# Kernel optimization log

Measured on AMD Instinct MI355X. Metric: run time of the kernel, lower is better.

## Reference

```python
import jax, jax.numpy as jnp
import numpy as np

N0 = N1 = N2 = N3 = 8          # input_shape
R = 8                           # input_ranks (rank_i)
L = 8                           # link_ranks (ring bond dims)
OR = 64                         # output_rank
OF = 1024                       # output_features
B = 4096                        # batch
STD = 0.09                      # ~calculate_std() for this config


def setup_inputs() -> dict:
    key = jax.random.key(0)
    ks = jax.random.split(key, 9)
    x = jax.random.normal(ks[0], (B, N0, N1, N2, N3), dtype=jnp.float32)
    # factor_i: (n_i, link_left, link_right, rank_i)
    f0 = jax.random.normal(ks[1], (N0, L, L, R), dtype=jnp.float32) * STD
    f1 = jax.random.normal(ks[2], (N1, L, L, R), dtype=jnp.float32) * STD
    f2 = jax.random.normal(ks[3], (N2, L, L, R), dtype=jnp.float32) * STD
    f3 = jax.random.normal(ks[4], (N3, L, L, R), dtype=jnp.float32) * STD
    core = jax.random.normal(ks[5], (R, R, R, R, OR), dtype=jnp.float32) * STD
    out_factor = jax.random.normal(ks[6], (OR, OF), dtype=jnp.float32) * STD
    bound = 1.0 / np.sqrt(N0 * N1 * N2 * N3)
    bias = jax.random.uniform(ks[7], (OF,), dtype=jnp.float32, minval=-bound, maxval=bound)
    return {"x": x, "f0": f0, "f1": f1, "f2": f2, "f3": f3,
            "core": core, "out_factor": out_factor, "bias": bias}


def _tr_weight(f0, f1, f2, f3, core, out_factor):
    # Contract the tensor-ring (factors + core + output factor) into the
    # effective weight W[n0,n1,n2,n3,out]. Contraction order chosen so every
    # intermediate stays small; result equals tn.contractors.greedy output.
    # core axes: p=r0, q=r1, s=r2, t=r3, o=out_rank; links a,b,c,d close the ring.
    t1 = jnp.einsum('iabp,pqsto->iabqsto', f0, core)      # [n0,L,L,r1,r2,r3,or]
    t2 = jnp.einsum('jbcq,iabqsto->ijacsto', f1, t1)      # [n0,n1,L,L,r2,r3,or]
    t3 = jnp.einsum('kcds,ijacsto->ijkadto', f2, t2)      # [n0,n1,n2,L,L,r3,or]
    t4 = jnp.einsum('ldat,ijkadto->ijklo', f3, t3)        # ring trace -> [n0..n3,or]
    return jnp.einsum('ijklo,of->ijklf', t4, out_factor)  # [n0,n1,n2,n3,out]


def reference(x, f0, f1, f2, f3, core, out_factor, bias):
    W = _tr_weight(f0, f1, f2, f3, core, out_factor)      # [8,8,8,8,1024]
    out = jnp.einsum('bijkl,ijklf->bf', x, W)             # [B, out_features]
    return out + bias
```

## Files before the change

kernel.cpp:

```cpp
#include <hip/hip_runtime.h>


#define WS_NEED ((size_t)25231360 * 4)

typedef __attribute__((ext_vector_type(8))) short short8v;
typedef __attribute__((ext_vector_type(4))) float f32x4;

__device__ inline unsigned short f2bf(float f) {
  unsigned u = __builtin_bit_cast(unsigned, f);
  u += 0x7FFFu + ((u >> 16) & 1u);
  return (unsigned short)(u >> 16);
}
__device__ inline float bf2f(unsigned short h) {
  return __builtin_bit_cast(float, (unsigned)h << 16);
}


__global__ __launch_bounds__(256) void k_build(const float* __restrict__ f0,
                                               const float* __restrict__ f1,
                                               const float* __restrict__ f2,
                                               const float* __restrict__ f3,
                                               float* __restrict__ G01,
                                               float* __restrict__ G23) {
  int bb = blockIdx.x, tid = threadIdx.x;
  __shared__ float lu[512], lv[512];
  bool is01 = bb < 64;
  int pairi = is01 ? bb : bb - 64;
  int iA = pairi >> 3, iB = pairi & 7;
  const float* fu = is01 ? f0 : f2;
  const float* fv = is01 ? f1 : f3;
  if (tid < 128)
    reinterpret_cast<float4*>(lu)[tid] = reinterpret_cast<const float4*>(fu + iA * 512)[tid];
  else
    reinterpret_cast<float4*>(lv)[tid - 128] = reinterpret_cast<const float4*>(fv + iB * 512)[tid - 128];
  __syncthreads();
  float* dst = is01 ? G01 : G23;
#pragma unroll
  for (int r = 0; r < 16; ++r) {
    int idx = r * 256 + tid;
    int uv = idx >> 6, pq = idx & 63;
    int a = uv >> 3, c = uv & 7, p = pq >> 3, q = pq & 7;
    float acc = 0.f;
    if (is01) {
#pragma unroll
      for (int b = 0; b < 8; ++b)
        acc = fmaf(lu[a * 64 + b * 8 + p], lv[b * 64 + c * 8 + q], acc);
    } else {
#pragma unroll
      for (int d = 0; d < 8; ++d)
        acc = fmaf(lu[c * 64 + d * 8 + p], lv[d * 64 + a * 8 + q], acc);
    }
    dst[pairi * 4096 + idx] = acc;
  }
}


__global__ __launch_bounds__(256) void k_packs(const float* __restrict__ G01,
                                               const float* __restrict__ G23,
                                               const float* __restrict__ core,
                                               const float* __restrict__ OF_,
                                               unsigned short* __restrict__ G01p,
                                               unsigned short* __restrict__ CP,
                                               unsigned short* __restrict__ G23p,
                                               unsigned short* __restrict__ OFp) {
  int bb = blockIdx.x, tid = threadIdx.x;
  __shared__ float ls[8192];
  if (bb < 64) {
    int ij = bb;
#pragma unroll
    for (int r = 0; r < 4; ++r)
      reinterpret_cast<float4*>(ls)[r * 256 + tid] =
          reinterpret_cast<const float4*>(G01 + ij * 4096)[r * 256 + tid];
    __syncthreads();
    short8v* dst = reinterpret_cast<short8v*>(G01p);
#pragma unroll
    for (int it = 0; it < 2; ++it) {
      int item = it * 256 + tid;
      int ks = item >> 8, mf = (item >> 6) & 3, l = item & 63;
      short8v hi, lo;
#pragma unroll
      for (int j = 0; j < 8; ++j) {
        float v = ls[(mf * 16 + (l & 15)) * 64 + ks * 32 + 8 * (l >> 4) + j];
        unsigned short h = f2bf(v);
        hi[j] = (short)h; lo[j] = (short)f2bf(v - bf2f(h));
      }
      size_t base = ((((size_t)ij * 2 + ks) * 4 + mf) * 2) * 64 + l;
      dst[base] = hi; dst[base + 64] = lo;
    }
  } else if (bb < 128) {
    int st = bb - 64;
#pragma unroll
    for (int r = 0; r < 4; ++r) {
      int f4 = r * 256 + tid;
      reinterpret_cast<float4*>(ls)[f4] =
          reinterpret_cast<const float4*>(core)[(f4 >> 4) * 1024 + st * 16 + (f4 & 15)];
    }
    __syncthreads();
    short8v* dst = reinterpret_cast<short8v*>(CP);
#pragma unroll
    for (int it = 0; it < 2; ++it) {
      int item = it * 256 + tid;
      int ks = item >> 8, nf = (item >> 6) & 3, l = item & 63;
      short8v hi, lo;
#pragma unroll
      for (int j = 0; j < 8; ++j) {
        float v = ls[(ks * 32 + 8 * (l >> 4) + j) * 64 + nf * 16 + (l & 15)];
        unsigned short h = f2bf(v);
        hi[j] = (short)h; lo[j] = (short)f2bf(v - bf2f(h));
      }
      size_t base = ((((size_t)st * 2 + ks) * 4 + nf) * 2) * 64 + l;
      dst[base] = hi; dst[base + 64] = lo;
    }
  } else if (bb < 256) {
    int ks = bb - 128;
    int st = ks >> 1, acb = (ks & 1) * 32;
#pragma unroll
    for (int r = 0; r < 8; ++r) {
      int idx = r * 256 + tid;
      ls[idx] = G23[(idx >> 5) * 4096 + (acb + (idx & 31)) * 64 + st];
    }
    __syncthreads();
    short8v* dst = reinterpret_cast<short8v*>(G23p);
    int mf = tid >> 6, l = tid & 63;
    short8v hi, lo;
#pragma unroll
    for (int j = 0; j < 8; ++j) {
      float v = ls[(mf * 16 + (l & 15)) * 32 + 8 * (l >> 4) + j];
      unsigned short h = f2bf(v);
      hi[j] = (short)h; lo[j] = (short)f2bf(v - bf2f(h));
    }
    size_t base = (((size_t)ks * 4 + mf) * 2) * 64 + l;
    dst[base] = hi; dst[base + 64] = lo;
  } else {
    int g = bb - 256;
#pragma unroll
    for (int it = 0; it < 8; ++it) {
      int f4 = it * 256 + tid;
      reinterpret_cast<float4*>(ls)[f4] =
          reinterpret_cast<const float4*>(OF_)[(f4 >> 5) * 256 + g * 32 + (f4 & 31)];
    }
    __syncthreads();
    short8v* dst = reinterpret_cast<short8v*>(OFp);
#pragma unroll
    for (int it = 0; it < 4; ++it) {
      int item = it * 256 + tid;
      int nfl = item >> 7, ks = (item >> 6) & 1, l = item & 63;
      short8v hi, lo;
#pragma unroll
      for (int j = 0; j < 8; ++j) {
        float v = ls[(ks * 32 + 8 * (l >> 4) + j) * 128 + nfl * 16 + (l & 15)];
        unsigned short h = f2bf(v);
        hi[j] = (short)h; lo[j] = (short)f2bf(v - bf2f(h));
      }
      int nfg = g * 8 + nfl;
      size_t base = (((size_t)nfg * 2 + ks) * 2) * 64 + l;
      dst[base] = hi; dst[base + 64] = lo;
    }
  }
}


__global__ __launch_bounds__(256) void k_dmat(const unsigned short* __restrict__ G01p,
                                              const unsigned short* __restrict__ CP,
                                              unsigned short* __restrict__ Dp) {
  int bid = blockIdx.x;
  int ij = bid >> 6, st = bid & 63;
  int w = threadIdx.x >> 6, l = threadIdx.x & 63;
  const short8v* gp = reinterpret_cast<const short8v*>(G01p);
  const short8v* cp = reinterpret_cast<const short8v*>(CP);
  short8v ah0 = gp[((((size_t)ij * 2 + 0) * 4 + w) * 2) * 64 + l];
  short8v al0 = gp[((((size_t)ij * 2 + 0) * 4 + w) * 2) * 64 + 64 + l];
  short8v ah1 = gp[((((size_t)ij * 2 + 1) * 4 + w) * 2) * 64 + l];
  short8v al1 = gp[((((size_t)ij * 2 + 1) * 4 + w) * 2) * 64 + 64 + l];
  f32x4 acc[4];
#pragma unroll
  for (int nf = 0; nf < 4; ++nf) acc[nf] = (f32x4){0.f, 0.f, 0.f, 0.f};
#pragma unroll
  for (int nf = 0; nf < 4; ++nf) {
    short8v bh0 = cp[((((size_t)st * 2 + 0) * 4 + nf) * 2) * 64 + l];
    short8v bl0 = cp[((((size_t)st * 2 + 0) * 4 + nf) * 2) * 64 + 64 + l];
    short8v bh1 = cp[((((size_t)st * 2 + 1) * 4 + nf) * 2) * 64 + l];
    short8v bl1 = cp[((((size_t)st * 2 + 1) * 4 + nf) * 2) * 64 + 64 + l];
    acc[nf] = __builtin_amdgcn_mfma_f32_16x16x32_bf16(ah0, bh0, acc[nf], 0, 0, 0);
    acc[nf] = __builtin_amdgcn_mfma_f32_16x16x32_bf16(al0, bh0, acc[nf], 0, 0, 0);
    acc[nf] = __builtin_amdgcn_mfma_f32_16x16x32_bf16(ah0, bl0, acc[nf], 0, 0, 0);
    acc[nf] = __builtin_amdgcn_mfma_f32_16x16x32_bf16(ah1, bh1, acc[nf], 0, 0, 0);
    acc[nf] = __builtin_amdgcn_mfma_f32_16x16x32_bf16(al1, bh1, acc[nf], 0, 0, 0);
    acc[nf] = __builtin_amdgcn_mfma_f32_16x16x32_bf16(ah1, bl1, acc[nf], 0, 0, 0);
  }
  __shared__ float lds[64 * 66];
#pragma unroll
  for (int nf = 0; nf < 4; ++nf)
#pragma unroll
    for (int r = 0; r < 4; ++r)
      lds[(w * 16 + 4 * (l >> 4) + r) * 66 + nf * 16 + (l & 15)] = acc[nf][r];
  __syncthreads();
  short8v* dst = reinterpret_cast<short8v*>(Dp);
#pragma unroll
  for (int it = 0; it < 2; ++it) {
    int item = it * 256 + threadIdx.x;
    int a2 = item >> 8, nf = (item >> 6) & 3, l2 = item & 63;
    short8v hi, lo;
#pragma unroll
    for (int j = 0; j < 8; ++j) {
      float v = lds[(a2 * 32 + 8 * (l2 >> 4) + j) * 66 + nf * 16 + (l2 & 15)];
      unsigned short hh = f2bf(v);
      hi[j] = (short)hh; lo[j] = (short)f2bf(v - bf2f(hh));
    }
    int ks = st * 2 + a2;
    size_t base = ((((size_t)ij * 128 + ks) * 4 + nf) * 2) * 64 + l2;
    dst[base] = hi; dst[base + 64] = lo;
  }
}


__global__ __launch_bounds__(256) void k_t4mm(const unsigned short* __restrict__ G23p,
                                              const unsigned short* __restrict__ Dp,
                                              float* __restrict__ T4part) {
  int bid = blockIdx.x;
  int ij = bid >> 3, kc = bid & 7;
  int w = threadIdx.x >> 6, l = threadIdx.x & 63;
  const short8v* ga = reinterpret_cast<const short8v*>(G23p);
  const short8v* gb = reinterpret_cast<const short8v*>(Dp);
  f32x4 acc[4];
#pragma unroll
  for (int nf = 0; nf < 4; ++nf) acc[nf] = (f32x4){0.f, 0.f, 0.f, 0.f};
#pragma unroll 2
  for (int ks = kc * 16; ks < kc * 16 + 16; ++ks) {
    size_t abase = (((size_t)ks * 4 + w) * 2) * 64 + l;
    short8v ah = ga[abase], al = ga[abase + 64];
#pragma unroll
    for (int nf = 0; nf < 4; ++nf) {
      size_t bbase = ((((size_t)ij * 128 + ks) * 4 + nf) * 2) * 64 + l;
      short8v bh = gb[bbase], bl = gb[bbase + 64];
      acc[nf] = __builtin_amdgcn_mfma_f32_16x16x32_bf16(ah, bh, acc[nf], 0, 0, 0);
      acc[nf] = __builtin_amdgcn_mfma_f32_16x16x32_bf16(al, bh, acc[nf], 0, 0, 0);
      acc[nf] = __builtin_amdgcn_mfma_f32_16x16x32_bf16(ah, bl, acc[nf], 0, 0, 0);
    }
  }
#pragma unroll
  for (int nf = 0; nf < 4; ++nf)
#pragma unroll
    for (int r = 0; r < 4; ++r) {
      int row = w * 16 + 4 * (l >> 4) + r;
      T4part[(((size_t)kc * 64 + ij) * 64 + row) * 64 + nf * 16 + (l & 15)] = acc[nf][r];
    }
}


__global__ __launch_bounds__(256) void k_pack2(const float* __restrict__ T4part,
                                               unsigned short* __restrict__ Bp) {
  int kb = blockIdx.x, tid = threadIdx.x;
  __shared__ float ls[2048];
  f32x4 a0 = {0.f, 0.f, 0.f, 0.f}, a1 = a0;
#pragma unroll
  for (int kc = 0; kc < 8; ++kc) {
    const f32x4* src = reinterpret_cast<const f32x4*>(T4part + (size_t)kc * 262144 + kb * 2048);
    a0 += src[tid];
    a1 += src[256 + tid];
  }
  reinterpret_cast<f32x4*>(ls)[tid] = a0;
  reinterpret_cast<f32x4*>(ls)[256 + tid] = a1;
  __syncthreads();
  short8v* dst = reinterpret_cast<short8v*>(Bp);
  int nf = tid >> 6, l = tid & 63;
  short8v hi, lo;
#pragma unroll
  for (int j = 0; j < 8; ++j) {
    float v = ls[(8 * (l >> 4) + j) * 64 + nf * 16 + (l & 15)];
    unsigned short h = f2bf(v);
    hi[j] = (short)h; lo[j] = (short)f2bf(v - bf2f(h));
  }
  size_t base = (size_t)kb * 512 + (nf * 2) * 64 + l;
  dst[base] = hi; dst[base + 64] = lo;
}


__global__ __launch_bounds__(256) void k_ymm(const float* __restrict__ x,
                                             const unsigned short* __restrict__ Bp,
                                             float* __restrict__ Ypart) {
  int mt = blockIdx.x >> 4, kc = blockIdx.x & 15;
  int w = threadIdx.x >> 6, l = threadIdx.x & 63;
  int kg = l >> 4, lm = l & 15;
  const float4* xp = reinterpret_cast<const float4*>(
      x + (size_t)(mt * 64 + w * 16 + lm) * 4096 + kc * 256 + kg * 8);
  f32x4 acc0 = {0.f, 0.f, 0.f, 0.f}, acc1 = acc0, acc2 = acc0, acc3 = acc0;
#pragma unroll 1
  for (int s = 0; s < 8; ++s) {
    float4 xa = xp[s * 8], xb = xp[s * 8 + 1];
    float xs[8] = {xa.x, xa.y, xa.z, xa.w, xb.x, xb.y, xb.z, xb.w};
    short8v ah, al;
#pragma unroll
    for (int j = 0; j < 8; ++j) {
      unsigned u = __builtin_bit_cast(unsigned, xs[j]);
      unsigned short h = (unsigned short)(u >> 16);
      ah[j] = (short)h;
      float lo = xs[j] - bf2f(h);
      al[j] = (short)(__builtin_bit_cast(unsigned, lo) >> 16);
    }
    const short8v* bp = reinterpret_cast<const short8v*>(Bp + (size_t)(kc * 8 + s) * 4096) + l;
    short8v bh0 = bp[0],   bl0 = bp[64];
    short8v bh1 = bp[128], bl1 = bp[192];
    short8v bh2 = bp[256], bl2 = bp[320];
    short8v bh3 = bp[384], bl3 = bp[448];
    acc0 = __builtin_amdgcn_mfma_f32_16x16x32_bf16(ah, bh0, acc0, 0, 0, 0);
    acc1 = __builtin_amdgcn_mfma_f32_16x16x32_bf16(ah, bh1, acc1, 0, 0, 0);
    acc2 = __builtin_amdgcn_mfma_f32_16x16x32_bf16(ah, bh2, acc2, 0, 0, 0);
    acc3 = __builtin_amdgcn_mfma_f32_16x16x32_bf16(ah, bh3, acc3, 0, 0, 0);
    acc0 = __builtin_amdgcn_mfma_f32_16x16x32_bf16(al, bh0, acc0, 0, 0, 0);
    acc1 = __builtin_amdgcn_mfma_f32_16x16x32_bf16(al, bh1, acc1, 0, 0, 0);
    acc2 = __builtin_amdgcn_mfma_f32_16x16x32_bf16(al, bh2, acc2, 0, 0, 0);
    acc3 = __builtin_amdgcn_mfma_f32_16x16x32_bf16(al, bh3, acc3, 0, 0, 0);
    acc0 = __builtin_amdgcn_mfma_f32_16x16x32_bf16(ah, bl0, acc0, 0, 0, 0);
    acc1 = __builtin_amdgcn_mfma_f32_16x16x32_bf16(ah, bl1, acc1, 0, 0, 0);
    acc2 = __builtin_amdgcn_mfma_f32_16x16x32_bf16(ah, bl2, acc2, 0, 0, 0);
    acc3 = __builtin_amdgcn_mfma_f32_16x16x32_bf16(ah, bl3, acc3, 0, 0, 0);
  }
  float* yb = Ypart + (size_t)kc * 262144 + (size_t)(mt * 64 + w * 16) * 64;
#pragma unroll
  for (int r = 0; r < 4; ++r) {
    yb[(kg * 4 + r) * 64 + 0  + lm] = acc0[r];
    yb[(kg * 4 + r) * 64 + 16 + lm] = acc1[r];
    yb[(kg * 4 + r) * 64 + 32 + lm] = acc2[r];
    yb[(kg * 4 + r) * 64 + 48 + lm] = acc3[r];
  }
}


__global__ __launch_bounds__(256) void k_out4(const float* __restrict__ Ypart,
                                              const unsigned short* __restrict__ OFp,
                                              const float* __restrict__ bias,
                                              float* __restrict__ out) {
  int mt16 = blockIdx.x;
  int tid = threadIdx.x;
  __shared__ float ls[1024];
  {
    f32x4 a = {0.f, 0.f, 0.f, 0.f};
#pragma unroll
    for (int kc = 0; kc < 16; ++kc)
      a += *reinterpret_cast<const f32x4*>(Ypart + (size_t)kc * 262144 + (size_t)mt16 * 1024 + tid * 4);
    *reinterpret_cast<f32x4*>(ls + tid * 4) = a;
  }
  __syncthreads();
  int w = tid >> 6, l = tid & 63;
  short8v ya0, yl0, ya1, yl1;
#pragma unroll
  for (int j = 0; j < 8; ++j) {
    float v0 = ls[(l & 15) * 64 + 0  + 8 * (l >> 4) + j];
    float v1 = ls[(l & 15) * 64 + 32 + 8 * (l >> 4) + j];
    unsigned short h0 = (unsigned short)(__builtin_bit_cast(unsigned, v0) >> 16);
    unsigned short h1 = (unsigned short)(__builtin_bit_cast(unsigned, v1) >> 16);
    ya0[j] = (short)h0; yl0[j] = (short)(__builtin_bit_cast(unsigned, v0 - bf2f(h0)) >> 16);
    ya1[j] = (short)h1; yl1[j] = (short)(__builtin_bit_cast(unsigned, v1 - bf2f(h1)) >> 16);
  }
  const short8v* op = reinterpret_cast<const short8v*>(OFp);
#pragma unroll 4
  for (int nf = 0; nf < 16; ++nf) {
    int nfg = w * 16 + nf;
    size_t bb = (((size_t)nfg * 2) * 2) * 64 + l;
    short8v bh0 = op[bb], bl0 = op[bb + 64], bh1 = op[bb + 128], bl1 = op[bb + 192];
    f32x4 acc = {0.f, 0.f, 0.f, 0.f};
    acc = __builtin_amdgcn_mfma_f32_16x16x32_bf16(ya0, bh0, acc, 0, 0, 0);
    acc = __builtin_amdgcn_mfma_f32_16x16x32_bf16(yl0, bh0, acc, 0, 0, 0);
    acc = __builtin_amdgcn_mfma_f32_16x16x32_bf16(ya0, bl0, acc, 0, 0, 0);
    acc = __builtin_amdgcn_mfma_f32_16x16x32_bf16(ya1, bh1, acc, 0, 0, 0);
    acc = __builtin_amdgcn_mfma_f32_16x16x32_bf16(yl1, bh1, acc, 0, 0, 0);
    acc = __builtin_amdgcn_mfma_f32_16x16x32_bf16(ya1, bl1, acc, 0, 0, 0);
    float bv = bias[nfg * 16 + (l & 15)];
#pragma unroll
    for (int r = 0; r < 4; ++r)
      out[(size_t)(mt16 * 16 + 4 * (l >> 4) + r) * 1024 + nfg * 16 + (l & 15)] = acc[r] + bv;
  }
}


__global__ __launch_bounds__(256) void k_t4(const float* __restrict__ A,
                                            const float* __restrict__ B,
                                            const float* __restrict__ core,
                                            float* __restrict__ T4) {
  int bid = blockIdx.x;
  int ij = bid >> 4, kl0 = (bid & 15) * 4;
  __shared__ float lA[4096];
  __shared__ float lS[4][4096];
  int tid = threadIdx.x;
#pragma unroll
  for (int r = 0; r < 4; ++r)
    reinterpret_cast<float4*>(lA)[r * 256 + tid] =
        reinterpret_cast<const float4*>(A + ij * 4096)[r * 256 + tid];
  __syncthreads();
  int pq0 = (tid >> 4) << 2;
  int st04 = tid & 15;
#pragma unroll 1
  for (int m = 0; m < 4; ++m) {
    const float4* Bp = reinterpret_cast<const float4*>(B + (kl0 + m) * 4096);
    float acc[4][4] = {{0.f}};
    for (int ac = 0; ac < 64; ++ac) {
      float4 av = reinterpret_cast<float4*>(lA)[ac * 16 + (pq0 >> 2)];
      float4 bv = Bp[ac * 16 + st04];
      float au[4] = {av.x, av.y, av.z, av.w};
      float bu[4] = {bv.x, bv.y, bv.z, bv.w};
#pragma unroll
      for (int u = 0; u < 4; ++u)
#pragma unroll
        for (int v = 0; v < 4; ++v)
          acc[u][v] = fmaf(au[u], bu[v], acc[u][v]);
    }
    float4* S4 = reinterpret_cast<float4*>(lS[m]);
#pragma unroll
    for (int u = 0; u < 4; ++u)
      S4[(pq0 + u) * 16 + st04] = make_float4(acc[u][0], acc[u][1], acc[u][2], acc[u][3]);
  }
  __syncthreads();
  int o44 = tid & 15, seg = tid >> 4;
  const float4* c4 = reinterpret_cast<const float4*>(core);
  float4 r0 = {0, 0, 0, 0}, r1 = r0, r2 = r0, r3 = r0;
  for (int n = 0; n < 256; ++n) {
    int midx = seg * 256 + n;
    float4 cv = c4[midx * 16 + o44];
    float s0 = lS[0][midx], s1 = lS[1][midx], s2 = lS[2][midx], s3 = lS[3][midx];
    r0.x = fmaf(s0, cv.x, r0.x); r0.y = fmaf(s0, cv.y, r0.y);
    r0.z = fmaf(s0, cv.z, r0.z); r0.w = fmaf(s0, cv.w, r0.w);
    r1.x = fmaf(s1, cv.x, r1.x); r1.y = fmaf(s1, cv.y, r1.y);
    r1.z = fmaf(s1, cv.z, r1.z); r1.w = fmaf(s1, cv.w, r1.w);
    r2.x = fmaf(s2, cv.x, r2.x); r2.y = fmaf(s2, cv.y, r2.y);
    r2.z = fmaf(s2, cv.z, r2.z); r2.w = fmaf(s2, cv.w, r2.w);
    r3.x = fmaf(s3, cv.x, r3.x); r3.y = fmaf(s3, cv.y, r3.y);
    r3.z = fmaf(s3, cv.z, r3.z); r3.w = fmaf(s3, cv.w, r3.w);
  }
  float4* red = reinterpret_cast<float4*>(lA);
  red[(seg * 4 + 0) * 16 + o44] = r0;
  red[(seg * 4 + 1) * 16 + o44] = r1;
  red[(seg * 4 + 2) * 16 + o44] = r2;
  red[(seg * 4 + 3) * 16 + o44] = r3;
  __syncthreads();
  int m2 = tid >> 6, o = tid & 63;
  float t = 0.f;
#pragma unroll
  for (int s2 = 0; s2 < 16; ++s2) t += lA[(s2 * 4 + m2) * 64 + o];
  T4[(ij * 64 + kl0 + m2) * 64 + o] = t;
}

__global__ __launch_bounds__(256) void k_y(const float* __restrict__ x,
                                           const float* __restrict__ T4,
                                           float* __restrict__ Y) {
  int b0 = blockIdx.x * 16;
  __shared__ float lx[1024];
  int tid = threadIdx.x;
  int o = tid & 63, rg = tid >> 6;
  float acc0 = 0.f, acc1 = 0.f, acc2 = 0.f, acc3 = 0.f;
  const float4* lx4 = reinterpret_cast<const float4*>(lx);
  for (int kc = 0; kc < 4096; kc += 64) {
    __syncthreads();
    reinterpret_cast<float4*>(lx)[tid] =
        *reinterpret_cast<const float4*>(x + (b0 + (tid >> 4)) * 4096 + kc + (tid & 15) * 4);
    __syncthreads();
#pragma unroll 4
    for (int kk = 0; kk < 64; kk += 4) {
      float c0 = T4[(kc + kk + 0) * 64 + o];
      float c1 = T4[(kc + kk + 1) * 64 + o];
      float c2 = T4[(kc + kk + 2) * 64 + o];
      float c3 = T4[(kc + kk + 3) * 64 + o];
      float4 xv;
      xv = lx4[(rg * 4 + 0) * 16 + (kk >> 2)];
      acc0 = fmaf(xv.x, c0, fmaf(xv.y, c1, fmaf(xv.z, c2, fmaf(xv.w, c3, acc0))));
      xv = lx4[(rg * 4 + 1) * 16 + (kk >> 2)];
      acc1 = fmaf(xv.x, c0, fmaf(xv.y, c1, fmaf(xv.z, c2, fmaf(xv.w, c3, acc1))));
      xv = lx4[(rg * 4 + 2) * 16 + (kk >> 2)];
      acc2 = fmaf(xv.x, c0, fmaf(xv.y, c1, fmaf(xv.z, c2, fmaf(xv.w, c3, acc2))));
      xv = lx4[(rg * 4 + 3) * 16 + (kk >> 2)];
      acc3 = fmaf(xv.x, c0, fmaf(xv.y, c1, fmaf(xv.z, c2, fmaf(xv.w, c3, acc3))));
    }
  }
  Y[(b0 + rg * 4 + 0) * 64 + o] = acc0;
  Y[(b0 + rg * 4 + 1) * 64 + o] = acc1;
  Y[(b0 + rg * 4 + 2) * 64 + o] = acc2;
  Y[(b0 + rg * 4 + 3) * 64 + o] = acc3;
}

__global__ __launch_bounds__(256) void k_out(const float* __restrict__ Y,
                                             const float* __restrict__ OF_,
                                             const float* __restrict__ bias,
                                             float* __restrict__ out) {
  int b0 = blockIdx.x * 16;
  int tid = threadIdx.x;
  __shared__ float lY[1024];
  reinterpret_cast<float4*>(lY)[tid] =
      *reinterpret_cast<const float4*>(Y + (b0 + (tid >> 4)) * 64 + (tid & 15) * 4);
  __syncthreads();
  float4 acc[16];
#pragma unroll
  for (int r = 0; r < 16; ++r) acc[r] = make_float4(0.f, 0.f, 0.f, 0.f);
  for (int oo = 0; oo < 64; ++oo) {
    float4 w = *reinterpret_cast<const float4*>(OF_ + oo * 1024 + tid * 4);
#pragma unroll
    for (int r = 0; r < 16; ++r) {
      float yv = lY[r * 64 + oo];
      acc[r].x = fmaf(yv, w.x, acc[r].x);
      acc[r].y = fmaf(yv, w.y, acc[r].y);
      acc[r].z = fmaf(yv, w.z, acc[r].z);
      acc[r].w = fmaf(yv, w.w, acc[r].w);
    }
  }
  float4 bv = *reinterpret_cast<const float4*>(bias + tid * 4);
#pragma unroll
  for (int r = 0; r < 16; ++r) {
    float4 v = acc[r];
    v.x += bv.x; v.y += bv.y; v.z += bv.z; v.w += bv.w;
    *reinterpret_cast<float4*>(out + (b0 + r) * 1024 + tid * 4) = v;
  }
}


extern "C" void kernel_launch(void* const* d_in, const int* in_sizes, int n_in,
                              void* d_out, int out_size, void* d_ws, size_t ws_size,
                              hipStream_t stream) {
  const float* x    = (const float*)d_in[0];
  const float* f0   = (const float*)d_in[1];
  const float* f1   = (const float*)d_in[2];
  const float* f2   = (const float*)d_in[3];
  const float* f3   = (const float*)d_in[4];
  const float* core = (const float*)d_in[5];
  const float* ofac = (const float*)d_in[6];
  const float* bias = (const float*)d_in[7];
  float* out = (float*)d_out;
  float* ws = (float*)d_ws;

  float* G01 = ws;
  float* G23 = ws + 262144;

  k_build<<<128, 256, 0, stream>>>(f0, f1, f2, f3, G01, G23);

  if (ws_size >= WS_NEED) {
    unsigned short* G01p = (unsigned short*)(ws + 524288);
    unsigned short* CP   = (unsigned short*)(ws + 786432);
    unsigned short* G23p = (unsigned short*)(ws + 1310720);
    unsigned short* Bp   = (unsigned short*)(ws + 1835008);
    unsigned short* OFp  = (unsigned short*)(ws + 2097152);
    float* T4part = ws + 2162688;
    float* Ypart  = ws + 4259840;
    unsigned short* Dp = (unsigned short*)(ws + 8454144);

    k_packs<<<264, 256, 0, stream>>>(G01, G23, core, ofac, G01p, CP, G23p, OFp);
    k_dmat<<<4096, 256, 0, stream>>>(G01p, CP, Dp);
    k_t4mm<<<512, 256, 0, stream>>>(G23p, Dp, T4part);
    k_pack2<<<128, 256, 0, stream>>>(T4part, Bp);
    k_ymm<<<1024, 256, 0, stream>>>(x, Bp, Ypart);
    k_out4<<<256, 256, 0, stream>>>(Ypart, OFp, bias, out);
  } else {
    float* T4 = ws + 524288;
    float* Yb = ws + 786432;
    k_t4<<<1024, 256, 0, stream>>>(G01, G23, core, T4);
    k_y<<<256, 256, 0, stream>>>(x, T4, Yb);
    k_out<<<256, 256, 0, stream>>>(Yb, ofac, bias, out);
  }
}
```

Baseline: 178.7 us.

## Fuse D-matrix build into T4 GEMM via LDS, eliminating Dp workspace

Merges k_dmat and k_t4mm into one kernel, k_t4f. Each block now computes its slice of the intermediate D matrix with MFMA, splits it into hi/lo bf16 in LDS, and consumes it right away in the T4 accumulation. This removes the large Dp global round trip, about 64 MB written and then read, along with one kernel launch, and shrinks the workspace requirement. In exchange there are only 512 blocks with a serialized 8-step loop and two barriers per step, which lowers parallelism and latency hiding compared with the 4096-block k_dmat.

```diff
diff --git a/kernel.cpp b/kernel.cpp
--- a/kernel.cpp
+++ b/kernel.cpp
@@ -1,7 +1,7 @@
 #include <hip/hip_runtime.h>
 
 
-#define WS_NEED ((size_t)25231360 * 4)
+#define WS_NEED ((size_t)7929856 * 4)
 
 typedef __attribute__((ext_vector_type(8))) short short8v;
 typedef __attribute__((ext_vector_type(4))) float f32x4;
@@ -160,82 +160,80 @@
 }
 
 
-__global__ __launch_bounds__(256) void k_dmat(const unsigned short* __restrict__ G01p,
-                                              const unsigned short* __restrict__ CP,
-                                              unsigned short* __restrict__ Dp) {
+__global__ __launch_bounds__(256) void k_t4f(const unsigned short* __restrict__ G01p,
+                                             const unsigned short* __restrict__ CP,
+                                             const unsigned short* __restrict__ G23p,
+                                             float* __restrict__ T4part) {
   int bid = blockIdx.x;
-  int ij = bid >> 6, st = bid & 63;
-  int w = threadIdx.x >> 6, l = threadIdx.x & 63;
+  int ij = bid >> 3, stc = bid & 7;
+  int tid = threadIdx.x;
+  int w = tid >> 6, l = tid & 63;
   const short8v* gp = reinterpret_cast<const short8v*>(G01p);
   const short8v* cp = reinterpret_cast<const short8v*>(CP);
-  short8v ah0 = gp[((((size_t)ij * 2 + 0) * 4 + w) * 2) * 64 + l];
-  short8v al0 = gp[((((size_t)ij * 2 + 0) * 4 + w) * 2) * 64 + 64 + l];
-  short8v ah1 = gp[((((size_t)ij * 2 + 1) * 4 + w) * 2) * 64 + l];
-  short8v al1 = gp[((((size_t)ij * 2 + 1) * 4 + w) * 2) * 64 + 64 + l];
-  f32x4 acc[4];
-#pragma unroll
-  for (int nf = 0; nf < 4; ++nf) acc[nf] = (f32x4){0.f, 0.f, 0.f, 0.f};
-#pragma unroll
-  for (int nf = 0; nf < 4; ++nf) {
-    short8v bh0 = cp[((((size_t)st * 2 + 0) * 4 + nf) * 2) * 64 + l];
-    short8v bl0 = cp[((((size_t)st * 2 + 0) * 4 + nf) * 2) * 64 + 64 + l];
-    short8v bh1 = cp[((((size_t)st * 2 + 1) * 4 + nf) * 2) * 64 + l];
-    short8v bl1 = cp[((((size_t)st * 2 + 1) * 4 + nf) * 2) * 64 + 64 + l];
-    acc[nf] = __builtin_amdgcn_mfma_f32_16x16x32_bf16(ah0, bh0, acc[nf], 0, 0, 0);
-    acc[nf] = __builtin_amdgcn_mfma_f32_16x16x32_bf16(al0, bh0, acc[nf], 0, 0, 0);
-    acc[nf] = __builtin_amdgcn_mfma_f32_16x16x32_bf16(ah0, bl0, acc[nf], 0, 0, 0);
-    acc[nf] = __builtin_amdgcn_mfma_f32_16x16x32_bf16(ah1, bh1, acc[nf], 0, 0, 0);
-    acc[nf] = __builtin_amdgcn_mfma_f32_16x16x32_bf16(al1, bh1, acc[nf], 0, 0, 0);
-    acc[nf] = __builtin_amdgcn_mfma_f32_16x16x32_bf16(ah1, bl1, acc[nf], 0, 0, 0);
-  }
-  __shared__ float lds[64 * 66];
-#pragma unroll
-  for (int nf = 0; nf < 4; ++nf)
-#pragma unroll
-    for (int r = 0; r < 4; ++r)
-      lds[(w * 16 + 4 * (l >> 4) + r) * 66 + nf * 16 + (l & 15)] = acc[nf][r];
-  __syncthreads();
-  short8v* dst = reinterpret_cast<short8v*>(Dp);
-#pragma unroll
-  for (int it = 0; it < 2; ++it) {
-    int item = it * 256 + threadIdx.x;
-    int a2 = item >> 8, nf = (item >> 6) & 3, l2 = item & 63;
-    short8v hi, lo;
-#pragma unroll
-    for (int j = 0; j < 8; ++j) {
-      float v = lds[(a2 * 32 + 8 * (l2 >> 4) + j) * 66 + nf * 16 + (l2 & 15)];
-      unsigned short hh = f2bf(v);
-      hi[j] = (short)hh; lo[j] = (short)f2bf(v - bf2f(hh));
-    }
-    int ks = st * 2 + a2;
-    size_t base = ((((size_t)ij * 128 + ks) * 4 + nf) * 2) * 64 + l2;
-    dst[base] = hi; dst[base + 64] = lo;
-  }
-}
-
-
-__global__ __launch_bounds__(256) void k_t4mm(const unsigned short* __restrict__ G23p,
-                                              const unsigned short* __restrict__ Dp,
-                                              float* __restrict__ T4part) {
-  int bid = blockIdx.x;
-  int ij = bid >> 3, kc = bid & 7;
-  int w = threadIdx.x >> 6, l = threadIdx.x & 63;
   const short8v* ga = reinterpret_cast<const short8v*>(G23p);
-  const short8v* gb = reinterpret_cast<const short8v*>(Dp);
-  f32x4 acc[4];
-#pragma unroll
-  for (int nf = 0; nf < 4; ++nf) acc[nf] = (f32x4){0.f, 0.f, 0.f, 0.f};
-#pragma unroll 2
-  for (int ks = kc * 16; ks < kc * 16 + 16; ++ks) {
-    size_t abase = (((size_t)ks * 4 + w) * 2) * 64 + l;
-    short8v ah = ga[abase], al = ga[abase + 64];
+  short8v a0h = gp[((((size_t)ij * 2 + 0) * 4 + w) * 2) * 64 + l];
+  short8v a0l = gp[((((size_t)ij * 2 + 0) * 4 + w) * 2) * 64 + 64 + l];
+  short8v a1h = gp[((((size_t)ij * 2 + 1) * 4 + w) * 2) * 64 + l];
+  short8v a1l = gp[((((size_t)ij * 2 + 1) * 4 + w) * 2) * 64 + 64 + l];
+  __shared__ float Ef[64 * 66];
+  __shared__ short EB[8192];
+  short8v* EBv = reinterpret_cast<short8v*>(EB);
+  f32x4 accT[4];
+#pragma unroll
+  for (int nf = 0; nf < 4; ++nf) accT[nf] = (f32x4){0.f, 0.f, 0.f, 0.f};
+
+#pragma unroll 1
+  for (int si = 0; si < 8; ++si) {
+    int st = stc * 8 + si;
+    f32x4 accE[4];
+#pragma unroll
+    for (int nf = 0; nf < 4; ++nf) accE[nf] = (f32x4){0.f, 0.f, 0.f, 0.f};
 #pragma unroll
     for (int nf = 0; nf < 4; ++nf) {
-      size_t bbase = ((((size_t)ij * 128 + ks) * 4 + nf) * 2) * 64 + l;
-      short8v bh = gb[bbase], bl = gb[bbase + 64];
-      acc[nf] = __builtin_amdgcn_mfma_f32_16x16x32_bf16(ah, bh, acc[nf], 0, 0, 0);
-      acc[nf] = __builtin_amdgcn_mfma_f32_16x16x32_bf16(al, bh, acc[nf], 0, 0, 0);
-      acc[nf] = __builtin_amdgcn_mfma_f32_16x16x32_bf16(ah, bl, acc[nf], 0, 0, 0);
+      short8v bh0 = cp[((((size_t)st * 2 + 0) * 4 + nf) * 2) * 64 + l];
+      short8v bl0 = cp[((((size_t)st * 2 + 0) * 4 + nf) * 2) * 64 + 64 + l];
+      short8v bh1 = cp[((((size_t)st * 2 + 1) * 4 + nf) * 2) * 64 + l];
+      short8v bl1 = cp[((((size_t)st * 2 + 1) * 4 + nf) * 2) * 64 + 64 + l];
+      accE[nf] = __builtin_amdgcn_mfma_f32_16x16x32_bf16(a0h, bh0, accE[nf], 0, 0, 0);
+      accE[nf] = __builtin_amdgcn_mfma_f32_16x16x32_bf16(a0l, bh0, accE[nf], 0, 0, 0);
+      accE[nf] = __builtin_amdgcn_mfma_f32_16x16x32_bf16(a0h, bl0, accE[nf], 0, 0, 0);
+      accE[nf] = __builtin_amdgcn_mfma_f32_16x16x32_bf16(a1h, bh1, accE[nf], 0, 0, 0);
+      accE[nf] = __builtin_amdgcn_mfma_f32_16x16x32_bf16(a1l, bh1, accE[nf], 0, 0, 0);
+      accE[nf] = __builtin_amdgcn_mfma_f32_16x16x32_bf16(a1h, bl1, accE[nf], 0, 0, 0);
+    }
+#pragma unroll
+    for (int nf = 0; nf < 4; ++nf)
+#pragma unroll
+      for (int r = 0; r < 4; ++r)
+        Ef[(w * 16 + 4 * (l >> 4) + r) * 66 + nf * 16 + (l & 15)] = accE[nf][r];
+    __syncthreads();
+#pragma unroll
+    for (int it = 0; it < 2; ++it) {
+      int item = it * 256 + tid;
+      int kch = item >> 8, nf = (item >> 6) & 3, l2 = item & 63;
+      short8v hi, lo;
+#pragma unroll
+      for (int j = 0; j < 8; ++j) {
+        float v = Ef[(kch * 32 + 8 * (l2 >> 4) + j) * 66 + nf * 16 + (l2 & 15)];
+        unsigned short hh = f2bf(v);
+        hi[j] = (short)hh; lo[j] = (short)f2bf(v - bf2f(hh));
+      }
+      EBv[((kch * 4 + nf) * 2 + 0) * 64 + l2] = hi;
+      EBv[((kch * 4 + nf) * 2 + 1) * 64 + l2] = lo;
+    }
+    __syncthreads();
+#pragma unroll
+    for (int kch = 0; kch < 2; ++kch) {
+      size_t abase = ((((size_t)(st * 2 + kch)) * 4 + w) * 2) * 64 + l;
+      short8v ah = ga[abase], al = ga[abase + 64];
+#pragma unroll
+      for (int nf = 0; nf < 4; ++nf) {
+        short8v bh = EBv[((kch * 4 + nf) * 2 + 0) * 64 + l];
+        short8v bl = EBv[((kch * 4 + nf) * 2 + 1) * 64 + l];
+        accT[nf] = __builtin_amdgcn_mfma_f32_16x16x32_bf16(ah, bh, accT[nf], 0, 0, 0);
+        accT[nf] = __builtin_amdgcn_mfma_f32_16x16x32_bf16(al, bh, accT[nf], 0, 0, 0);
+        accT[nf] = __builtin_amdgcn_mfma_f32_16x16x32_bf16(ah, bl, accT[nf], 0, 0, 0);
+      }
     }
   }
 #pragma unroll
@@ -243,7 +241,7 @@
 #pragma unroll
     for (int r = 0; r < 4; ++r) {
       int row = w * 16 + 4 * (l >> 4) + r;
-      T4part[(((size_t)kc * 64 + ij) * 64 + row) * 64 + nf * 16 + (l & 15)] = acc[nf][r];
+      T4part[(((size_t)stc * 64 + ij) * 64 + row) * 64 + nf * 16 + (l & 15)] = accT[nf][r];
     }
 }
 
@@ -533,16 +531,14 @@
   if (ws_size >= WS_NEED) {
     unsigned short* G01p = (unsigned short*)(ws + 524288);
     unsigned short* CP   = (unsigned short*)(ws + 786432);
-    unsigned short* G23p = (unsigned short*)(ws + 1310720);
-    unsigned short* Bp   = (unsigned short*)(ws + 1835008);
-    unsigned short* OFp  = (unsigned short*)(ws + 2097152);
-    float* T4part = ws + 2162688;
-    float* Ypart  = ws + 4259840;
-    unsigned short* Dp = (unsigned short*)(ws + 8454144);
+    unsigned short* G23p = (unsigned short*)(ws + 1048576);
+    unsigned short* Bp   = (unsigned short*)(ws + 1310720);
+    unsigned short* OFp  = (unsigned short*)(ws + 1572864);
+    float* T4part = ws + 1638400;
+    float* Ypart  = ws + 3735552;
 
     k_packs<<<264, 256, 0, stream>>>(G01, G23, core, ofac, G01p, CP, G23p, OFp);
-    k_dmat<<<4096, 256, 0, stream>>>(G01p, CP, Dp);
-    k_t4mm<<<512, 256, 0, stream>>>(G23p, Dp, T4part);
+    k_t4f<<<512, 256, 0, stream>>>(G01p, CP, G23p, T4part);
     k_pack2<<<128, 256, 0, stream>>>(T4part, Bp);
     k_ymm<<<1024, 256, 0, stream>>>(x, Bp, Ypart);
     k_out4<<<256, 256, 0, stream>>>(Ypart, OFp, bias, out);
```

Measured after the change: 168.0 us. 6.0% less time.
